# Kernel optimization log

Hardware: AMD Instinct MI355X
Metric: run time of the kernel (lower is better)

The kernel has to match this reference:

```python
import jax, jax.numpy as jnp
import numpy as np

# ---- model hyperparams (from init_kwargs) ----
N_USERS = 200000
N_ITEMS = 100000
DIM = 64
NNZ = 3000000
BATCH = 4096
N_HOPS = 3          # context_hops
EPS = 0.1           # SimGCL perturbation magnitude
TEMP = 0.2          # tau
CL_RATE = 0.5       # lamb
DECAY = 1e-4        # l2


def setup_inputs() -> dict:
    key = jax.random.key(0)
    k = jax.random.split(key, 8)
    user_embed = (jax.random.normal(k[0], (N_USERS, DIM), dtype=jnp.float32) * 0.01)
    item_embed = (jax.random.normal(k[1], (N_ITEMS, DIM), dtype=jnp.float32) * 0.01)
    N = N_USERS + N_ITEMS
    # COO normalized adjacency (buffer, not a parameter in the torch module)
    adj_rows = jax.random.randint(k[2], (NNZ,), 0, N)
    adj_cols = jax.random.randint(k[3], (NNZ,), 0, N)
    adj_vals = jax.random.uniform(k[4], (NNZ,), dtype=jnp.float32) * 0.2
    # unique index batches (torch code calls torch.unique for the CL loss;
    # sampling without replacement makes skipping unique exact, since the
    # InfoNCE mean is permutation invariant)
    users = jax.random.permutation(k[5], N_USERS)[:BATCH].astype(jnp.int32)
    pos_items = jax.random.permutation(k[6], N_ITEMS)[:BATCH].astype(jnp.int32)
    neg_items = jax.random.randint(k[7], (BATCH,), 0, N_ITEMS)
    return {"user_embed": user_embed, "item_embed": item_embed,
            "adj_vals": adj_vals, "adj_rows": adj_rows, "adj_cols": adj_cols,
            "users": users, "pos_items": pos_items, "neg_items": neg_items}


def _spmm(vals, rows, cols, x):
    # torch.sparse.mm(A, x) with A in COO form: out[r] += v * x[c]
    return jax.ops.segment_sum(vals[:, None] * x[cols], rows, num_segments=x.shape[0])


def _gcn(user_embed, item_embed, vals, rows, cols, perturbed, key):
    ego = jnp.concatenate([user_embed, item_embed], axis=0)  # [N, D]
    acc = jnp.zeros_like(ego)
    for h in range(N_HOPS):
        ego = _spmm(vals, rows, cols, ego)
        if perturbed:
            noise = jax.random.uniform(jax.random.fold_in(key, h), ego.shape, dtype=ego.dtype)
            noise = noise / jnp.maximum(jnp.linalg.norm(noise, axis=-1, keepdims=True), 1e-12)
            ego = ego + jnp.sign(ego) * noise * EPS
        acc = acc + ego
    mean = acc / N_HOPS   # stack + mean over hops == running-sum / n_hops
    return mean[:N_USERS], mean[N_USERS:]


def _info_nce(v1, v2, temp):
    v1 = v1 / jnp.maximum(jnp.linalg.norm(v1, axis=1, keepdims=True), 1e-12)
    v2 = v2 / jnp.maximum(jnp.linalg.norm(v2, axis=1, keepdims=True), 1e-12)
    pos = jnp.exp(jnp.sum(v1 * v2, axis=-1) / temp)              # [B]
    ttl = jnp.sum(jnp.exp((v1 @ v2.T) / temp), axis=1)           # [B]
    return jnp.mean(-jnp.log(pos / ttl + 1e-5))


def reference(user_embed, item_embed, adj_vals, adj_rows, adj_cols, users, pos_items, neg_items):
    # --- recommendation branch (no perturbation) ---
    ru, ri = _gcn(user_embed, item_embed, adj_vals, adj_rows, adj_cols, False, jax.random.key(0))
    ue, pe, ne = ru[users], ri[pos_items], ri[neg_items]
    pos_score = jnp.sum(ue * pe, axis=1)
    neg_score = jnp.sum(ue * ne, axis=1)
    rec_loss = jnp.mean(-jnp.log(1e-5 + jax.nn.sigmoid(pos_score - neg_score)))
    reg_loss = DECAY * (jnp.linalg.norm(ue) + jnp.linalg.norm(pe))  # Frobenius norms
    # --- contrastive branch: two perturbed views of the whole GCN ---
    u1, i1 = _gcn(user_embed, item_embed, adj_vals, adj_rows, adj_cols, True, jax.random.key(101))
    u2, i2 = _gcn(user_embed, item_embed, adj_vals, adj_rows, adj_cols, True, jax.random.key(202))
    cl_loss = CL_RATE * (_info_nce(u1[users], u2[users], TEMP)
                         + _info_nce(i1[pos_items], i2[pos_items], TEMP))
    return rec_loss + reg_loss + cl_loss
```

## Files before the change

kernel.cpp:

```cpp
#include <hip/hip_runtime.h>
#include <stdint.h>

#define NUSERS  200000
#define NITEMS  100000
#define NTOT    300000
#define DIM     64
#define NU64    (NUSERS * DIM)
#define NNZC    3000000
#define BATCH   4096
#define B64     (BATCH * DIM)
#define EPSP    0.1f
#define INV_TEMP 5.0f
#define SCAN_ELEMS 1024
#define GELEMS ((size_t)7 * B64 + 2 * BATCH + 8)

#define BSHIFT 11
#define BROWS  (1 << BSHIFT)
#define NB     ((NTOT + BROWS - 1) / BROWS)
#define CHUNK  4096
#define NCHUNK ((NNZC + CHUNK - 1) / CHUNK)
#define NH     (NB * NCHUNK)
#define CASTB  ((NTOT * DIM) / 2048)

typedef short bf16x8 __attribute__((ext_vector_type(8)));
typedef float f32x4  __attribute__((ext_vector_type(4)));

__device__ __forceinline__ float b2f(unsigned short h) {
  return __uint_as_float(((uint32_t)h) << 16);
}
__device__ __forceinline__ unsigned short f2b(float f) {
  uint32_t b = __float_as_uint(f);
  uint32_t r = b + 0x7FFFu + ((b >> 16) & 1u);
  return (unsigned short)(r >> 16);
}

__device__ __forceinline__ uint32_t mix32(uint32_t h) {
  h ^= h >> 16; h *= 0x85EBCA6Bu;
  h ^= h >> 13; h *= 0xC2B2AE35u;
  h ^= h >> 16;
  return h;
}
__device__ __forceinline__ uint32_t noise_key(uint32_t seed, uint32_t hop) {
  return mix32(seed * 0x9E3779B9u + hop * 0x85EBCA6Bu + 0x1BD11BDAu);
}
__device__ __forceinline__ float fast_unif(uint32_t key, uint32_t e) {
  uint32_t h = mix32(key + e * 0x9E3779B9u);
  return __uint_as_float((h >> 9) | 0x3F800000u) - 1.0f;
}
__device__ __forceinline__ float n_ss4(uint32_t key, uint32_t rq, float4& u) {
  uint32_t h = mix32(key + rq * 0x9E3779B9u);
  u.x = ((float)(h & 255u)         + 0.5f) * (1.0f / 256.0f);
  u.y = ((float)((h >> 8) & 255u)  + 0.5f) * (1.0f / 256.0f);
  u.z = ((float)((h >> 16) & 255u) + 0.5f) * (1.0f / 256.0f);
  u.w = ((float)(h >> 24)          + 0.5f) * (1.0f / 256.0f);
  return u.x * u.x + u.y * u.y + u.z * u.z + u.w * u.w;
}

__device__ __forceinline__ float sgnf(float a) {
  return (a > 0.f) ? 1.f : ((a < 0.f) ? -1.f : 0.f);
}

__global__ __launch_bounds__(256) void partA_cast(
    const int* __restrict__ rows, int* __restrict__ Hcnt,
    const float* __restrict__ uemb, const float* __restrict__ iemb,
    unsigned short* __restrict__ X0) {
  int blk = blockIdx.x;
  if (blk >= NCHUNK) {
    int base = (blk - NCHUNK) * 2048 + threadIdx.x * 8;
    const float* src = (base < NU64) ? (uemb + base) : (iemb + (base - NU64));
    float4 f0 = ((const float4*)src)[0];
    float4 f1 = ((const float4*)src)[1];
    uint4 o;
    o.x = ((uint32_t)f2b(f0.y) << 16) | f2b(f0.x);
    o.y = ((uint32_t)f2b(f0.w) << 16) | f2b(f0.z);
    o.z = ((uint32_t)f2b(f1.y) << 16) | f2b(f1.x);
    o.w = ((uint32_t)f2b(f1.w) << 16) | f2b(f1.z);
    *(uint4*)(X0 + base) = o;
    return;
  }
  __shared__ int bc[256];
  int c = blk, t = threadIdx.x;
  bc[t] = 0;
  __syncthreads();
  int base = c * CHUNK;
  for (int i = t; i < CHUNK; i += 256) {
    int e = base + i;
    if (e < NNZC) atomicAdd(&bc[rows[e] >> BSHIFT], 1);
  }
  __syncthreads();
  if (t < NB) Hcnt[t * NCHUNK + c] = bc[t];
}

__global__ void scan_block(const int* __restrict__ cnt, int* __restrict__ out,
                           int* __restrict__ bsums, int n) {
  __shared__ int tmp[SCAN_ELEMS];
  int base = blockIdx.x * SCAN_ELEMS;
  int t = threadIdx.x;
  #pragma unroll
  for (int q = 0; q < 4; ++q) {
    int k = t + q * 256, i = base + k;
    tmp[k] = (i < n) ? cnt[i] : 0;
  }
  __syncthreads();
  for (int off = 1; off < SCAN_ELEMS; off <<= 1) {
    int v[4];
    #pragma unroll
    for (int q = 0; q < 4; ++q) {
      int k = t + q * 256;
      v[q] = (k >= off) ? tmp[k - off] : 0;
    }
    __syncthreads();
    #pragma unroll
    for (int q = 0; q < 4; ++q) tmp[t + q * 256] += v[q];
    __syncthreads();
  }
  #pragma unroll
  for (int q = 0; q < 4; ++q) {
    int k = t + q * 256, i = base + k;
    if (i < n) out[i] = (k == 0) ? 0 : tmp[k - 1];
  }
  if (t == 0) bsums[blockIdx.x] = tmp[SCAN_ELEMS - 1];
}

__global__ void scan_sums(int* __restrict__ bsums, int nb) {
  __shared__ int tmp[512];
  int t = threadIdx.x;
  tmp[t] = (t < nb) ? bsums[t] : 0;
  __syncthreads();
  for (int off = 1; off < 512; off <<= 1) {
    int v = (t >= off) ? tmp[t - off] : 0;
    __syncthreads();
    tmp[t] += v;
    __syncthreads();
  }
  if (t < nb) bsums[t] = (t == 0) ? 0 : tmp[t - 1];
}

__global__ void add_offsets(int* __restrict__ out, const int* __restrict__ bsums,
                            int n) {
  int i = blockIdx.x * blockDim.x + threadIdx.x;
  if (i < n) out[i] += bsums[i / SCAN_ELEMS];
}

__global__ void add_offsets_emit(int* __restrict__ vmap,
                                 const int* __restrict__ bsums,
                                 const int* __restrict__ vflag,
                                 int* __restrict__ vlist,
                                 int* __restrict__ nV) {
  int i = blockIdx.x * blockDim.x + threadIdx.x;
  if (i >= NTOT) return;
  int m = vmap[i] + bsums[i / SCAN_ELEMS];
  vmap[i] = m;
  if (vflag[i]) vlist[m] = i;
  if (i == NTOT - 1) nV[0] = m + vflag[i];
}

__global__ __launch_bounds__(256) void partB(const float* __restrict__ vals,
                                             const int* __restrict__ rows,
                                             const int* __restrict__ cols,
                                             const int* __restrict__ Hofs,
                                             int2* __restrict__ midp,
                                             int* __restrict__ midr) {
  __shared__ int2 stv[CHUNK];
  __shared__ int  str_[CHUNK];
  __shared__ int  cnt[256];
  __shared__ int  sc[256];
  __shared__ int  adj[NB];
  int c = blockIdx.x, t = threadIdx.x;
  cnt[t] = 0;
  __syncthreads();
  int base = c * CHUNK;
  for (int i = t; i < CHUNK; i += 256) {
    int e = base + i;
    if (e < NNZC) atomicAdd(&cnt[rows[e] >> BSHIFT], 1);
  }
  __syncthreads();
  sc[t] = cnt[t];
  __syncthreads();
  for (int off = 1; off < 256; off <<= 1) {
    int u = (t >= off) ? sc[t - off] : 0;
    __syncthreads();
    sc[t] += u;
    __syncthreads();
  }
  int excl = sc[t] - cnt[t];
  cnt[t] = excl;
  if (t < NB) adj[t] = Hofs[t * NCHUNK + c] - excl;
  __syncthreads();
  for (int i = t; i < CHUNK; i += 256) {
    int e = base + i;
    if (e < NNZC) {
      int r = rows[e];
      int b = r >> BSHIFT;
      int p = atomicAdd(&cnt[b], 1);
      stv[p] = make_int2(__float_as_int(vals[e]), cols[e] * DIM);
      str_[p] = r;
    }
  }
  __syncthreads();
  int n = NNZC - base;
  if (n > CHUNK) n = CHUNK;
  for (int p = t; p < n; p += 256) {
    int r = str_[p];
    int b = r >> BSHIFT;
    int dst = adj[b] + p;
    midp[dst] = stv[p];
    midr[dst] = r;
  }
}

__global__ __launch_bounds__(256) void partC(const int2* __restrict__ midp,
                                             const int* __restrict__ midr,
                                             const int* __restrict__ Hofs,
                                             int* __restrict__ rs,
                                             int2* __restrict__ pairs) {
  __shared__ int h[BROWS];
  __shared__ int tsum[256];
  int b = blockIdx.x, t = threadIdx.x;
  int row0 = b << BSHIFT;
  for (int i = t; i < BROWS; i += 256) h[i] = 0;
  __syncthreads();
  int s = Hofs[b * NCHUNK];
  int e = (b + 1 < NB) ? Hofs[(b + 1) * NCHUNK] : NNZC;
  for (int p = s + t; p < e; p += 256)
    atomicAdd(&h[midr[p] - row0], 1);
  __syncthreads();
  int loc[8], run = 0;
  #pragma unroll
  for (int k = 0; k < 8; ++k) { loc[k] = run; run += h[t * 8 + k]; }
  tsum[t] = run;
  __syncthreads();
  for (int off = 1; off < 256; off <<= 1) {
    int v = (t >= off) ? tsum[t - off] : 0;
    __syncthreads();
    tsum[t] += v;
    __syncthreads();
  }
  int baseT = (t == 0) ? 0 : tsum[t - 1];
  #pragma unroll
  for (int k = 0; k < 8; ++k) {
    int i = t * 8 + k;
    int pos = s + baseT + loc[k];
    if (row0 + i < NTOT) rs[row0 + i] = pos;
    h[i] = pos;
  }
  if (b == NB - 1 && t == 0) rs[NTOT] = NNZC;
  __syncthreads();
  for (int p = s + t; p < e; p += 256) {
    int r = midr[p];
    int2 v = midp[p];
    int pos = atomicAdd(&h[r - row0], 1);
    pairs[pos] = v;
  }
}

__global__ __launch_bounds__(256) void mark_v(const int* __restrict__ u,
                                              const int* __restrict__ p,
                                              const int* __restrict__ n,
                                              const int* __restrict__ rs,
                                              const int2* __restrict__ pairs,
                                              int* __restrict__ vflag) {
  int i = blockIdx.x * 256 + threadIdx.x;
  if (i >= 3 * BATCH) return;
  int v = (i < BATCH) ? u[i]
        : (i < 2 * BATCH) ? (NUSERS + p[i - BATCH])
        : (NUSERS + n[i - 2 * BATCH]);
  vflag[v] = 1;
  int s = rs[v], e = rs[v + 1];
  for (int j = s; j < e; ++j) vflag[(unsigned)pairs[j].y >> 6] = 1;
}

template <bool PERT>
__global__ __launch_bounds__(256) void spmm_hop(
    const int2* __restrict__ pairs, const int* __restrict__ rs,
    const unsigned short* __restrict__ x,
    unsigned short* __restrict__ y, uint32_t seed, uint32_t hop) {
  int tid  = threadIdx.x;
  int lane = tid & 63;
  int q    = lane & 15;
  int wave = (blockIdx.x * 256 + tid) >> 6;
  int r    = wave * 4 + (lane >> 4);
  int s    = rs[r];
  int e    = rs[r + 1];
  int q4 = q * 4;
  float a0[4] = {0.f, 0.f, 0.f, 0.f};
  for (int j = s; j < e; j += 8) {
    int2 p[8];
    #pragma unroll
    for (int k = 0; k < 8; ++k)
      p[k] = (j + k < e) ? pairs[j + k] : make_int2(0, 0);
    #pragma unroll
    for (int k = 0; k < 8; ++k) {
      float v = __int_as_float(p[k].x);
      unsigned o = (unsigned)(p[k].y + q4);
      ushort4 h = *(const ushort4*)(x + o);
      a0[0] = fmaf(v, b2f(h.x), a0[0]); a0[1] = fmaf(v, b2f(h.y), a0[1]);
      a0[2] = fmaf(v, b2f(h.z), a0[2]); a0[3] = fmaf(v, b2f(h.w), a0[3]);
    }
  }
  int ebase = r * 64 + q4;
  if (PERT) {
    uint32_t key = noise_key(seed, hop);
    float u[4], ss = 0.f;
    #pragma unroll
    for (int k = 0; k < 4; ++k) {
      u[k] = fast_unif(key, (uint32_t)(ebase + k));
      ss += u[k] * u[k];
    }
    #pragma unroll
    for (int msk = 1; msk < 16; msk <<= 1) ss += __shfl_xor(ss, msk);
    float sc = EPSP / fmaxf(sqrtf(ss), 1e-12f);
    #pragma unroll
    for (int k = 0; k < 4; ++k) a0[k] += sgnf(a0[k]) * u[k] * sc;
  }
  ushort4 st;
  st.x = f2b(a0[0]); st.y = f2b(a0[1]); st.z = f2b(a0[2]); st.w = f2b(a0[3]);
  *(ushort4*)(y + ebase) = st;
}

__global__ __launch_bounds__(256) void perturb3(
    const unsigned short* __restrict__ A,
    unsigned short* __restrict__ A1, unsigned short* __restrict__ A2) {
  const uint32_t k101 = noise_key(101u, 0u);
  const uint32_t k202 = noise_key(202u, 0u);
  int tid  = threadIdx.x;
  int lane = tid & 63;
  int q    = lane & 15;
  int wave = (blockIdx.x * 256 + tid) >> 6;
  int r    = wave * 4 + (lane >> 4);
  int ebase = r * 64 + q * 4;
  ushort4 h4 = *(const ushort4*)(A + ebase);
  float a[4] = {b2f(h4.x), b2f(h4.y), b2f(h4.z), b2f(h4.w)};
  float4 u1, u2;
  float s1 = n_ss4(k101, (uint32_t)(r * 16 + q), u1);
  float s2 = n_ss4(k202, (uint32_t)(r * 16 + q), u2);
  #pragma unroll
  for (int m = 1; m < 16; m <<= 1) {
    s1 += __shfl_xor(s1, m);
    s2 += __shfl_xor(s2, m);
  }
  float sc1 = EPSP / fmaxf(sqrtf(s1), 1e-12f);
  float sc2 = EPSP / fmaxf(sqrtf(s2), 1e-12f);
  float g0 = sgnf(a[0]), g1 = sgnf(a[1]), g2 = sgnf(a[2]), g3 = sgnf(a[3]);
  ushort4 o1, o2;
  o1.x = f2b(fmaf(g0 * u1.x, sc1, a[0]));
  o1.y = f2b(fmaf(g1 * u1.y, sc1, a[1]));
  o1.z = f2b(fmaf(g2 * u1.z, sc1, a[2]));
  o1.w = f2b(fmaf(g3 * u1.w, sc1, a[3]));
  o2.x = f2b(fmaf(g0 * u2.x, sc2, a[0]));
  o2.y = f2b(fmaf(g1 * u2.y, sc2, a[1]));
  o2.z = f2b(fmaf(g2 * u2.z, sc2, a[2]));
  o2.w = f2b(fmaf(g3 * u2.w, sc2, a[3]));
  *(ushort4*)(A1 + ebase) = o1;
  *(ushort4*)(A2 + ebase) = o2;
}

__global__ __launch_bounds__(256) void spmm_subz(
    const int2* __restrict__ pairs, const int* __restrict__ rs,
    const int* __restrict__ vlist, const int* __restrict__ nVp,
    const unsigned short* __restrict__ x0,
    const unsigned short* __restrict__ x1,
    const unsigned short* __restrict__ x2,
    unsigned short* __restrict__ y0, unsigned short* __restrict__ y1,
    unsigned short* __restrict__ y2) {
  int nV = nVp[0];
  if (blockIdx.x * 16 >= nV) return;
  int z = blockIdx.y;
  const unsigned short* x = (z == 0) ? x0 : ((z == 1) ? x1 : x2);
  unsigned short* y = (z == 0) ? y0 : ((z == 1) ? y1 : y2);
  int tid  = threadIdx.x;
  int lane = tid & 63;
  int q    = lane & 15;
  int wave = (blockIdx.x * 256 + tid) >> 6;
  int slot = wave * 4 + (lane >> 4);
  if (slot >= nV) return;
  int v = vlist[slot];
  int s = rs[v];
  int e = rs[v + 1];
  int q4 = q * 4;
  float a0[4] = {0.f, 0.f, 0.f, 0.f};
  for (int j = s; j < e; j += 8) {
    int2 p[8];
    #pragma unroll
    for (int k = 0; k < 8; ++k)
      p[k] = (j + k < e) ? pairs[j + k] : make_int2(0, 0);
    #pragma unroll
    for (int k = 0; k < 8; ++k) {
      float vv = __int_as_float(p[k].x);
      unsigned o = (unsigned)(p[k].y + q4);
      ushort4 h = *(const ushort4*)(x + o);
      a0[0] = fmaf(vv, b2f(h.x), a0[0]); a0[1] = fmaf(vv, b2f(h.y), a0[1]);
      a0[2] = fmaf(vv, b2f(h.z), a0[2]); a0[3] = fmaf(vv, b2f(h.w), a0[3]);
    }
  }
  if (z) {
    uint32_t key = noise_key((z == 1) ? 101u : 202u, 1u);
    int en = v * 64 + q4;
    float u[4], ss = 0.f;
    #pragma unroll
    for (int k = 0; k < 4; ++k) {
      u[k] = fast_unif(key, (uint32_t)(en + k));
      ss += u[k] * u[k];
    }
    #pragma unroll
    for (int msk = 1; msk < 16; msk <<= 1) ss += __shfl_xor(ss, msk);
    float sc = EPSP / fmaxf(sqrtf(ss), 1e-12f);
    #pragma unroll
    for (int k = 0; k < 4; ++k) a0[k] += sgnf(a0[k]) * u[k] * sc;
  }
  ushort4 st;
  st.x = f2b(a0[0]); st.y = f2b(a0[1]); st.z = f2b(a0[2]); st.w = f2b(a0[3]);
  *(ushort4*)(y + slot * 64 + q4) = st;
}

__global__ __launch_bounds__(256) void hop2g7(
    const int2* __restrict__ pairs, const int* __restrict__ rs,
    const unsigned short* __restrict__ Abuf,
    const unsigned short* __restrict__ B0,
    const unsigned short* __restrict__ B1,
    const unsigned short* __restrict__ B2,
    const int* __restrict__ vmap,
    const int* __restrict__ users, const int* __restrict__ pos,
    const int* __restrict__ neg,
    float* __restrict__ g, unsigned short* __restrict__ gb) {
  int by = blockIdx.y;
  int br = (by < 3) ? 0 : ((by < 5) ? 1 : 2);
  const int* idx = (by == 2) ? neg
                 : ((by == 1 || by == 4 || by == 6) ? pos : users);
  int base = (by == 0 || by == 3 || by == 5) ? 0 : NUSERS;
  float* o = g + (size_t)by * B64;
  const unsigned short* Bt = (br == 0) ? B0 : ((br == 1) ? B1 : B2);
  uint32_t seed = (br == 1) ? 101u : 202u;
  int tid  = threadIdx.x;
  int lane = tid & 63;
  int q    = lane & 15;
  int q4 = q * 4;
  int slot = blockIdx.x * 16 + (tid >> 6) * 4 + (lane >> 4);
  int row  = base + idx[slot];
  int s    = rs[row];
  int e    = rs[row + 1];
  float a0[4] = {0.f, 0.f, 0.f, 0.f};
  for (int j = s; j < e; j += 8) {
    int2 p[8];
    #pragma unroll
    for (int k = 0; k < 8; ++k)
      p[k] = (j + k < e) ? pairs[j + k] : make_int2(0, 0);
    int sl[8];
    #pragma unroll
    for (int k = 0; k < 8; ++k)
      sl[k] = vmap[(unsigned)p[k].y >> 6];
    #pragma unroll
    for (int k = 0; k < 8; ++k) {
      float v = __int_as_float(p[k].x);
      unsigned of = (unsigned)(sl[k] * DIM + q4);
      ushort4 h = *(const ushort4*)(Bt + of);
      a0[0] = fmaf(v, b2f(h.x), a0[0]); a0[1] = fmaf(v, b2f(h.y), a0[1]);
      a0[2] = fmaf(v, b2f(h.z), a0[2]); a0[3] = fmaf(v, b2f(h.w), a0[3]);
    }
  }
  if (br) {
    uint32_t key = noise_key(seed, 2u);
    int en = row * 64 + q4;
    float u[4], ss = 0.f;
    #pragma unroll
    for (int k = 0; k < 4; ++k) {
      u[k] = fast_unif(key, (uint32_t)(en + k));
      ss += u[k] * u[k];
    }
    #pragma unroll
    for (int msk = 1; msk < 16; msk <<= 1) ss += __shfl_xor(ss, msk);
    float sc = EPSP / fmaxf(sqrtf(ss), 1e-12f);
    #pragma unroll
    for (int k = 0; k < 4; ++k) a0[k] += sgnf(a0[k]) * u[k] * sc;
  }
  size_t rbA = (size_t)row * DIM + q4;
  size_t rbB = (size_t)vmap[row] * DIM + q4;
  ushort4 ha = *(const ushort4*)(Abuf + rbA);
  ushort4 hb = *(const ushort4*)(Bt + rbB);
  float af[4] = {b2f(ha.x), b2f(ha.y), b2f(ha.z), b2f(ha.w)};
  if (br) {
    uint32_t key0 = noise_key(seed, 0u);
    float4 u;
    float ssn = n_ss4(key0, (uint32_t)(row * 16 + q), u);
    #pragma unroll
    for (int m = 1; m < 16; m <<= 1) ssn += __shfl_xor(ssn, m);
    float scn = EPSP / fmaxf(sqrtf(ssn), 1e-12f);
    af[0] = fmaf(sgnf(af[0]) * u.x, scn, af[0]);
    af[1] = fmaf(sgnf(af[1]) * u.y, scn, af[1]);
    af[2] = fmaf(sgnf(af[2]) * u.z, scn, af[2]);
    af[3] = fmaf(sgnf(af[3]) * u.w, scn, af[3]);
  }
  float rv[4];
  rv[0] = (af[0] + b2f(hb.x)) + a0[0];
  rv[1] = (af[1] + b2f(hb.y)) + a0[1];
  rv[2] = (af[2] + b2f(hb.z)) + a0[2];
  rv[3] = (af[3] + b2f(hb.w)) + a0[3];
  if (br) {
    float ss = rv[0]*rv[0] + rv[1]*rv[1] + rv[2]*rv[2] + rv[3]*rv[3];
    #pragma unroll
    for (int msk = 1; msk < 16; msk <<= 1) ss += __shfl_xor(ss, msk);
    float inv = 1.0f / fmaxf(sqrtf(ss), 1e-12f);
    #pragma unroll
    for (int k = 0; k < 4; ++k) rv[k] *= inv;
  }
  int og = slot * 64 + q4;
  *(float4*)(o + og) = make_float4(rv[0], rv[1], rv[2], rv[3]);
  if (br) {
    unsigned short* ob = gb + (size_t)(by - 3) * B64;
    ushort4 sb;
    sb.x = f2b(rv[0]); sb.y = f2b(rv[1]); sb.z = f2b(rv[2]); sb.w = f2b(rv[3]);
    *(ushort4*)(ob + og) = sb;
  }
}

template <bool PERT>
__global__ __launch_bounds__(256) void spmm_sub(
    const int2* __restrict__ pairs, const int* __restrict__ rs,
    const int* __restrict__ vlist, const int* __restrict__ nVp,
    const unsigned short* __restrict__ x,
    unsigned short* __restrict__ y, uint32_t seed, uint32_t hop) {
  int nV = nVp[0];
  if (blockIdx.x * 16 >= nV) return;
  int tid  = threadIdx.x;
  int lane = tid & 63;
  int q    = lane & 15;
  int wave = (blockIdx.x * 256 + tid) >> 6;
  int slot = wave * 4 + (lane >> 4);
  if (slot >= nV) return;
  int v = vlist[slot];
  int s = rs[v];
  int e = rs[v + 1];
  int q4 = q * 4;
  float a0[4] = {0.f, 0.f, 0.f, 0.f};
  for (int j = s; j < e; j += 8) {
    int2 p[8];
    #pragma unroll
    for (int k = 0; k < 8; ++k)
      p[k] = (j + k < e) ? pairs[j + k] : make_int2(0, 0);
    #pragma unroll
    for (int k = 0; k < 8; ++k) {
      float vv = __int_as_float(p[k].x);
      unsigned o = (unsigned)(p[k].y + q4);
      ushort4 h = *(const ushort4*)(x + o);
      a0[0] = fmaf(vv, b2f(h.x), a0[0]); a0[1] = fmaf(vv, b2f(h.y), a0[1]);
      a0[2] = fmaf(vv, b2f(h.z), a0[2]); a0[3] = fmaf(vv, b2f(h.w), a0[3]);
    }
  }
  if (PERT) {
    uint32_t key = noise_key(seed, hop);
    int en = v * 64 + q4;
    float u[4], ss = 0.f;
    #pragma unroll
    for (int k = 0; k < 4; ++k) {
      u[k] = fast_unif(key, (uint32_t)(en + k));
      ss += u[k] * u[k];
    }
    #pragma unroll
    for (int msk = 1; msk < 16; msk <<= 1) ss += __shfl_xor(ss, msk);
    float sc = EPSP / fmaxf(sqrtf(ss), 1e-12f);
    #pragma unroll
    for (int k = 0; k < 4; ++k) a0[k] += sgnf(a0[k]) * u[k] * sc;
  }
  ushort4 st;
  st.x = f2b(a0[0]); st.y = f2b(a0[1]); st.z = f2b(a0[2]); st.w = f2b(a0[3]);
  *(ushort4*)(y + slot * 64 + q4) = st;
}

template <bool REVERT>
__global__ __launch_bounds__(256) void perturb(unsigned short* __restrict__ A,
                                               uint32_t seedRm, uint32_t seedAdd) {
  int tid  = threadIdx.x;
  int lane = tid & 63;
  int q    = lane & 15;
  int wave = (blockIdx.x * 256 + tid) >> 6;
  int r    = wave * 4 + (lane >> 4);
  int ebase = r * 64 + q * 4;
  ushort4 h4 = *(ushort4*)(A + ebase);
  float av[4] = {b2f(h4.x), b2f(h4.y), b2f(h4.z), b2f(h4.w)};
  if (REVERT) {
    uint32_t key = noise_key(seedRm, 0u);
    float4 u;
    float ss = n_ss4(key, (uint32_t)(r * 16 + q), u);
    #pragma unroll
    for (int msk = 1; msk < 16; msk <<= 1) ss += __shfl_xor(ss, msk);
    float sc = EPSP / fmaxf(sqrtf(ss), 1e-12f);
    av[0] -= sgnf(av[0]) * u.x * sc;
    av[1] -= sgnf(av[1]) * u.y * sc;
    av[2] -= sgnf(av[2]) * u.z * sc;
    av[3] -= sgnf(av[3]) * u.w * sc;
  }
  {
    uint32_t key = noise_key(seedAdd, 0u);
    float4 u;
    float ss = n_ss4(key, (uint32_t)(r * 16 + q), u);
    #pragma unroll
    for (int msk = 1; msk < 16; msk <<= 1) ss += __shfl_xor(ss, msk);
    float sc = EPSP / fmaxf(sqrtf(ss), 1e-12f);
    av[0] += sgnf(av[0]) * u.x * sc;
    av[1] += sgnf(av[1]) * u.y * sc;
    av[2] += sgnf(av[2]) * u.z * sc;
    av[3] += sgnf(av[3]) * u.w * sc;
  }
  ushort4 st;
  st.x = f2b(av[0]); st.y = f2b(av[1]); st.z = f2b(av[2]); st.w = f2b(av[3]);
  *(ushort4*)(A + ebase) = st;
}

template <bool PERT, bool NORM>
__global__ __launch_bounds__(256) void hop2g(
    const int2* __restrict__ pairs, const int* __restrict__ rs,
    const unsigned short* __restrict__ Abuf,
    const unsigned short* __restrict__ Bbuf,
    const int* __restrict__ vmap,
    const int* __restrict__ i0, const int* __restrict__ i1,
    const int* __restrict__ i2,
    float* __restrict__ o0, float* __restrict__ o1, float* __restrict__ o2,
    unsigned short* __restrict__ ob0, unsigned short* __restrict__ ob1,
    int b0, int b1, int b2, uint32_t seed) {
  int seg = blockIdx.y;
  const int* idx = (seg == 0) ? i0 : ((seg == 1) ? i1 : i2);
  float* o = (seg == 0) ? o0 : ((seg == 1) ? o1 : o2);
  unsigned short* ob = (seg == 0) ? ob0 : ob1;
  int base = (seg == 0) ? b0 : ((seg == 1) ? b1 : b2);
  int tid  = threadIdx.x;
  int lane = tid & 63;
  int q    = lane & 15;
  int q4 = q * 4;
  int slot = blockIdx.x * 16 + (tid >> 6) * 4 + (lane >> 4);
  int row  = base + idx[slot];
  int s    = rs[row];
  int e    = rs[row + 1];
  float a0[4] = {0.f, 0.f, 0.f, 0.f};
  for (int j = s; j < e; j += 8) {
    int2 p[8];
    #pragma unroll
    for (int k = 0; k < 8; ++k)
      p[k] = (j + k < e) ? pairs[j + k] : make_int2(0, 0);
    int sl[8];
    #pragma unroll
    for (int k = 0; k < 8; ++k)
      sl[k] = vmap[(unsigned)p[k].y >> 6];
    #pragma unroll
    for (int k = 0; k < 8; ++k) {
      float v = __int_as_float(p[k].x);
      unsigned of = (unsigned)(sl[k] * DIM + q4);
      ushort4 h = *(const ushort4*)(Bbuf + of);
      a0[0] = fmaf(v, b2f(h.x), a0[0]); a0[1] = fmaf(v, b2f(h.y), a0[1]);
      a0[2] = fmaf(v, b2f(h.z), a0[2]); a0[3] = fmaf(v, b2f(h.w), a0[3]);
    }
  }
  if (PERT) {
    uint32_t key = noise_key(seed, 2u);
    int en = row * 64 + q4;
    float u[4], ss = 0.f;
    #pragma unroll
    for (int k = 0; k < 4; ++k) {
      u[k] = fast_unif(key, (uint32_t)(en + k));
      ss += u[k] * u[k];
    }
    #pragma unroll
    for (int msk = 1; msk < 16; msk <<= 1) ss += __shfl_xor(ss, msk);
    float sc = EPSP / fmaxf(sqrtf(ss), 1e-12f);
    #pragma unroll
    for (int k = 0; k < 4; ++k) a0[k] += sgnf(a0[k]) * u[k] * sc;
  }
  size_t rbA = (size_t)row * DIM + q4;
  size_t rbB = (size_t)vmap[row] * DIM + q4;
  ushort4 ha = *(const ushort4*)(Abuf + rbA);
  ushort4 hb = *(const ushort4*)(Bbuf + rbB);
  float rv[4];
  rv[0] = (b2f(ha.x) + b2f(hb.x)) + a0[0];
  rv[1] = (b2f(ha.y) + b2f(hb.y)) + a0[1];
  rv[2] = (b2f(ha.z) + b2f(hb.z)) + a0[2];
  rv[3] = (b2f(ha.w) + b2f(hb.w)) + a0[3];
  if (NORM) {
    float ss = rv[0]*rv[0] + rv[1]*rv[1] + rv[2]*rv[2] + rv[3]*rv[3];
    #pragma unroll
    for (int msk = 1; msk < 16; msk <<= 1) ss += __shfl_xor(ss, msk);
    float inv = 1.0f / fmaxf(sqrtf(ss), 1e-12f);
    #pragma unroll
    for (int k = 0; k < 4; ++k) rv[k] *= inv;
  }
  int og = slot * 64 + q4;
  *(float4*)(o + og) = make_float4(rv[0], rv[1], rv[2], rv[3]);
  if (NORM) {
    ushort4 sb;
    sb.x = f2b(rv[0]); sb.y = f2b(rv[1]); sb.z = f2b(rv[2]); sb.w = f2b(rv[3]);
    *(ushort4*)(ob + og) = sb;
  }
}

__global__ __launch_bounds__(256) void nce_ttl_mfma(
    const unsigned short* __restrict__ u1b, const unsigned short* __restrict__ u2b,
    float* __restrict__ tu,
    const unsigned short* __restrict__ w1b, const unsigned short* __restrict__ w2b,
    float* __restrict__ tw) {
  const unsigned short* V1 = (blockIdx.z == 0) ? u1b : w1b;
  const unsigned short* V2 = (blockIdx.z == 0) ? u2b : w2b;
  float* ttl = (blockIdx.z == 0) ? tu : tw;
  int tid  = threadIdx.x;
  int lane = tid & 63;
  int wv   = tid >> 6;
  int lr   = lane & 15;
  int lk   = (lane >> 4) * 8;
  int m0   = blockIdx.x * 64 + wv * 16;
  bf16x8 a0 = *(const bf16x8*)(V1 + (size_t)(m0 + lr) * DIM + lk);
  bf16x8 a1 = *(const bf16x8*)(V1 + (size_t)(m0 + lr) * DIM + 32 + lk);
  float rowsum[4] = {0.f, 0.f, 0.f, 0.f};
  int n0 = blockIdx.y * 256;
  for (int ch = 0; ch < 4; ++ch) {
    int nc = n0 + ch * 64;
    #pragma unroll
    for (int nt = 0; nt < 4; ++nt) {
      int col = nc + nt * 16 + lr;
      bf16x8 b0 = *(const bf16x8*)(V2 + (size_t)col * DIM + lk);
      bf16x8 b1 = *(const bf16x8*)(V2 + (size_t)col * DIM + 32 + lk);
      f32x4 c = {0.f, 0.f, 0.f, 0.f};
      c = __builtin_amdgcn_mfma_f32_16x16x32_bf16(a0, b0, c, 0, 0, 0);
      c = __builtin_amdgcn_mfma_f32_16x16x32_bf16(a1, b1, c, 0, 0, 0);
      #pragma unroll
      for (int rr = 0; rr < 4; ++rr)
        rowsum[rr] += __expf(c[rr] * INV_TEMP);
    }
  }
  #pragma unroll
  for (int rr = 0; rr < 4; ++rr) {
    float s = rowsum[rr];
    #pragma unroll
    for (int m = 1; m < 16; m <<= 1) s += __shfl_xor(s, m);
    rowsum[rr] = s;
  }
  if (lr == 0) {
    int rbase = m0 + (lane >> 4) * 4;
    #pragma unroll
    for (int rr = 0; rr < 4; ++rr)
      atomicAdd(&ttl[rbase + rr], rowsum[rr]);
  }
}

__global__ __launch_bounds__(256) void nce_final2(const float* __restrict__ g,
                                                  const float* __restrict__ ttl_u,
                                                  float* __restrict__ acc) {
  int by = blockIdx.y;
  const float* v1 = g + (size_t)(3 + by) * B64;
  const float* v2 = g + (size_t)(5 + by) * B64;
  const float* ttl = ttl_u + by * BATCH;
  float* a = acc + 3 + by;
  __shared__ float red[4];
  int tid = threadIdx.x, lane = tid & 63, wv = tid >> 6;
  int gw = blockIdx.x * 4 + wv;
  float l = 0.f;
  for (int r = gw; r < BATCH; r += 256) {
    int gid = r * 64 + lane;
    float p = v1[gid] * v2[gid];
    #pragma unroll
    for (int m = 32; m; m >>= 1) p += __shfl_xor(p, m);
    if (lane == 0) l += -logf(__expf(p * INV_TEMP) / ttl[r] + 1e-5f);
  }
  if (lane == 0) red[wv] = l;
  __syncthreads();
  if (tid == 0) atomicAdd(a, red[0] + red[1] + red[2] + red[3]);
}

__global__ __launch_bounds__(256) void rec_kernel(const float* __restrict__ ue,
                                                  const float* __restrict__ pe,
                                                  const float* __restrict__ ne,
                                                  float* __restrict__ acc) {
  __shared__ float red[3][4];
  int tid = threadIdx.x, lane = tid & 63, wv = tid >> 6;
  int gw = blockIdx.x * 4 + wv;
  const float third = 1.0f / 3.0f;
  float l = 0.f, su = 0.f, sp = 0.f;
  for (int r = gw; r < BATCH; r += 256) {
    int gid = r * 64 + lane;
    float u = ue[gid] * third, p = pe[gid] * third, n = ne[gid] * third;
    float ps = u * p, ns = u * n;
    su += u * u; sp += p * p;
    #pragma unroll
    for (int m = 32; m; m >>= 1) { ps += __shfl_xor(ps, m); ns += __shfl_xor(ns, m); }
    if (lane == 0) {
      float sig = 1.0f / (1.0f + __expf(-(ps - ns)));
      l += -logf(1e-5f + sig);
    }
  }
  #pragma unroll
  for (int m = 32; m; m >>= 1) { su += __shfl_xor(su, m); sp += __shfl_xor(sp, m); }
  if (lane == 0) { red[0][wv] = l; red[1][wv] = su; red[2][wv] = sp; }
  __syncthreads();
  if (tid == 0) {
    atomicAdd(acc + 0, red[0][0] + red[0][1] + red[0][2] + red[0][3]);
    atomicAdd(acc + 1, red[1][0] + red[1][1] + red[1][2] + red[1][3]);
    atomicAdd(acc + 2, red[2][0] + red[2][1] + red[2][2] + red[2][3]);
  }
}

__global__ void finalize_kernel(const float* __restrict__ acc, float* __restrict__ out) {
  out[0] = acc[0] * (1.0f / BATCH)
         + 1e-4f * (sqrtf(acc[1]) + sqrtf(acc[2]))
         + 0.5f * (acc[3] + acc[4]) * (1.0f / BATCH);
}

extern "C" void kernel_launch(void* const* d_in, const int* in_sizes, int n_in,
                              void* d_out, int out_size, void* d_ws, size_t ws_size,
                              hipStream_t stream) {
  (void)in_sizes; (void)n_in; (void)out_size;
  const float* user_embed = (const float*)d_in[0];
  const float* item_embed = (const float*)d_in[1];
  const float* adj_vals   = (const float*)d_in[2];
  const int*   adj_rows   = (const int*)d_in[3];
  const int*   adj_cols   = (const int*)d_in[4];
  const int*   users      = (const int*)d_in[5];
  const int*   pos_items  = (const int*)d_in[6];
  const int*   neg_items  = (const int*)d_in[7];
  float* out = (float*)d_out;

  const size_t bufElems = (size_t)NTOT * DIM;

  unsigned short* A  = (unsigned short*)d_ws;
  unsigned short* B0 = A + bufElems;
  int2*  pairs = (int2*)(B0 + bufElems);
  float* g     = (float*)(pairs + NNZC);
  float* g_ue = g + 0 * (size_t)B64;
  float* g_pe = g + 1 * (size_t)B64;
  float* g_ne = g + 2 * (size_t)B64;
  float* g_u1 = g + 3 * (size_t)B64;
  float* g_i1 = g + 4 * (size_t)B64;
  float* g_u2 = g + 5 * (size_t)B64;
  float* g_i2 = g + 6 * (size_t)B64;
  float* ttl_u = g + 7 * (size_t)B64;
  float* ttl_i = ttl_u + BATCH;
  float* acc   = ttl_i + BATCH;
  int* rs     = (int*)(g + GELEMS);
  int* bsums  = rs + (NTOT + 1);
  int* vflag  = bsums + 512;
  int* vmap   = vflag + NTOT;
  int* vlist  = vmap + NTOT;
  int* nVd    = vlist + NTOT;
  unsigned short* gb = (unsigned short*)(((uintptr_t)(nVd + 1) + 31) & ~(uintptr_t)31);
  unsigned short* g_u1b = gb + 0 * (size_t)B64;
  unsigned short* g_i1b = gb + 1 * (size_t)B64;
  unsigned short* g_u2b = gb + 2 * (size_t)B64;
  unsigned short* g_i2b = gb + 3 * (size_t)B64;

  uintptr_t endBase = (uintptr_t)(gb + 4 * (size_t)B64);
  unsigned short* B1 = (unsigned short*)((endBase + 15) & ~(uintptr_t)15);
  unsigned short* B2 = B1 + bufElems;
  unsigned short* A1 = B2 + bufElems;
  unsigned short* A2 = A1 + bufElems;
  size_t need_full = (size_t)((uintptr_t)(A2 + bufElems) - (uintptr_t)d_ws);
  const bool fused = (ws_size == 0) || (ws_size >= need_full);

  int2* midp = (int2*)A;
  int*  midr = (int*)(midp + NNZC);
  int*  Hcnt = midr + NNZC;
  int*  Hofs = Hcnt + NH;
  unsigned short* X0 = B0;

  hipMemsetAsync(ttl_u, 0, (2 * BATCH + 8) * sizeof(float), stream);
  hipMemsetAsync(vflag, 0, NTOT * sizeof(int), stream);

  partA_cast<<<NCHUNK + CASTB, 256, 0, stream>>>(adj_rows, Hcnt,
                                                 user_embed, item_embed, X0);
  const int nhb = (NH + SCAN_ELEMS - 1) / SCAN_ELEMS;
  scan_block<<<nhb, 256, 0, stream>>>(Hcnt, Hofs, bsums, NH);
  scan_sums<<<1, 512, 0, stream>>>(bsums, nhb);
  add_offsets<<<(NH + 255) / 256, 256, 0, stream>>>(Hofs, bsums, NH);
  partB<<<NCHUNK, 256, 0, stream>>>(adj_vals, adj_rows, adj_cols, Hofs, midp, midr);
  partC<<<NB, 256, 0, stream>>>(midp, midr, Hofs, rs, pairs);

  mark_v<<<(3 * BATCH + 255) / 256, 256, 0, stream>>>(
      users, pos_items, neg_items, rs, pairs, vflag);
  const int nvb = (NTOT + SCAN_ELEMS - 1) / SCAN_ELEMS;
  scan_block<<<nvb, 256, 0, stream>>>(vflag, vmap, bsums, NTOT);
  scan_sums<<<1, 512, 0, stream>>>(bsums, nvb);
  add_offsets_emit<<<(NTOT + 255) / 256, 256, 0, stream>>>(vmap, bsums, vflag,
                                                           vlist, nVd);

  const int spmm_blocks = NTOT / 16;

  spmm_hop<false><<<spmm_blocks, 256, 0, stream>>>(pairs, rs, X0, A, 0u, 0u);

  if (fused) {
    perturb3<<<spmm_blocks, 256, 0, stream>>>(A, A1, A2);
    dim3 subz(spmm_blocks, 3);
    spmm_subz<<<subz, 256, 0, stream>>>(pairs, rs, vlist, nVd,
                                        A, A1, A2, B0, B1, B2);
    dim3 h2g7(BATCH / 16, 7);
    hop2g7<<<h2g7, 256, 0, stream>>>(pairs, rs, A, B0, B1, B2, vmap,
                                     users, pos_items, neg_items, g, gb);
  } else {
    dim3 h2g3(BATCH / 16, 3), h2g2(BATCH / 16, 2);
    spmm_sub<false><<<spmm_blocks, 256, 0, stream>>>(
        pairs, rs, vlist, nVd, A, B0, 0u, 0u);
    hop2g<false, false><<<h2g3, 256, 0, stream>>>(
        pairs, rs, A, B0, vmap, users, pos_items, neg_items,
        g_ue, g_pe, g_ne, nullptr, nullptr, 0, NUSERS, NUSERS, 0u);
    perturb<false><<<spmm_blocks, 256, 0, stream>>>(A, 0u, 101u);
    spmm_sub<true><<<spmm_blocks, 256, 0, stream>>>(
        pairs, rs, vlist, nVd, A, B0, 101u, 1u);
    hop2g<true, true><<<h2g2, 256, 0, stream>>>(
        pairs, rs, A, B0, vmap, users, pos_items, nullptr,
        g_u1, g_i1, nullptr, g_u1b, g_i1b, 0, NUSERS, 0, 101u);
    perturb<true><<<spmm_blocks, 256, 0, stream>>>(A, 101u, 202u);
    spmm_sub<true><<<spmm_blocks, 256, 0, stream>>>(
        pairs, rs, vlist, nVd, A, B0, 202u, 1u);
    hop2g<true, true><<<h2g2, 256, 0, stream>>>(
        pairs, rs, A, B0, vmap, users, pos_items, nullptr,
        g_u2, g_i2, nullptr, g_u2b, g_i2b, 0, NUSERS, 0, 202u);
  }

  rec_kernel<<<64, 256, 0, stream>>>(g_ue, g_pe, g_ne, acc);
  dim3 nce_grid(BATCH / 64, BATCH / 256, 2);
  nce_ttl_mfma<<<nce_grid, 256, 0, stream>>>(g_u1b, g_u2b, ttl_u,
                                             g_i1b, g_i2b, ttl_i);
  dim3 nfin(64, 2);
  nce_final2<<<nfin, 256, 0, stream>>>(g, ttl_u, acc);
  finalize_kernel<<<1, 1, 0, stream>>>(acc, out);
}
```

Measured before the change: 567.3 us.

## Fuse hop-1 SpMM with perturbation, merge scans, memsets and loss kernels

Folds the two memsets into extra blocks of the cast/count kernel and merges the single-block bsums scan into the add-offset kernels, with each block redundantly rescanning the block sums. The first-hop SpMM is fused with the dual perturbation so A is not re-read, and the rec and NCE final kernels are merged into one launch. B buffers are shrunk to a capacity BCAP for the subset of needed rows, reducing workspace. The intent is fewer launches and less memory traffic. The risks are silent truncation if the needed-row count exceeds BCAP, and redundant scan work in every block.

Measured after the change: 481.6 us. 15.1% less time.

```diff
diff --git a/kernel.cpp b/kernel.cpp
--- a/kernel.cpp
+++ b/kernel.cpp
@@ -13,6 +13,7 @@
 #define INV_TEMP 5.0f
 #define SCAN_ELEMS 1024
 #define GELEMS ((size_t)7 * B64 + 2 * BATCH + 8)
+#define BCAP   163840
 
 #define BSHIFT 11
 #define BROWS  (1 << BSHIFT)
@@ -21,6 +22,10 @@
 #define NCHUNK ((NNZC + CHUNK - 1) / CHUNK)
 #define NH     (NB * NCHUNK)
 #define CASTB  ((NTOT * DIM) / 2048)
+#define Z4V    (NTOT / 4)
+#define Z4T    ((2 * BATCH + 8) / 4)
+#define ZVB    ((Z4V + 511) / 512)
+#define ZTB    ((Z4T + 511) / 512)
 
 typedef short bf16x8 __attribute__((ext_vector_type(8)));
 typedef float f32x4  __attribute__((ext_vector_type(4)));
@@ -63,8 +68,25 @@
 __global__ __launch_bounds__(256) void partA_cast(
     const int* __restrict__ rows, int* __restrict__ Hcnt,
     const float* __restrict__ uemb, const float* __restrict__ iemb,
-    unsigned short* __restrict__ X0) {
+    unsigned short* __restrict__ X0,
+    int* __restrict__ vflag, float* __restrict__ ttlz) {
   int blk = blockIdx.x;
+  if (blk >= NCHUNK + CASTB + ZVB) {
+    int i4 = (blk - NCHUNK - CASTB - ZVB) * 512 + threadIdx.x;
+    float4 z = make_float4(0.f, 0.f, 0.f, 0.f);
+    if (i4 < Z4T) ((float4*)ttlz)[i4] = z;
+    i4 += 256;
+    if (i4 < Z4T) ((float4*)ttlz)[i4] = z;
+    return;
+  }
+  if (blk >= NCHUNK + CASTB) {
+    int i4 = (blk - NCHUNK - CASTB) * 512 + threadIdx.x;
+    int4 z = make_int4(0, 0, 0, 0);
+    if (i4 < Z4V) ((int4*)vflag)[i4] = z;
+    i4 += 256;
+    if (i4 < Z4V) ((int4*)vflag)[i4] = z;
+    return;
+  }
   if (blk >= NCHUNK) {
     int base = (blk - NCHUNK) * 2048 + threadIdx.x * 8;
     const float* src = (base < NU64) ? (uemb + base) : (iemb + (base - NU64));
@@ -122,37 +144,55 @@
   if (t == 0) bsums[blockIdx.x] = tmp[SCAN_ELEMS - 1];
 }
 
-__global__ void scan_sums(int* __restrict__ bsums, int nb) {
+__global__ void add_offsets_scan(int* __restrict__ out,
+                                 const int* __restrict__ bsums,
+                                 int n, int nb) {
   __shared__ int tmp[512];
   int t = threadIdx.x;
   tmp[t] = (t < nb) ? bsums[t] : 0;
+  tmp[t + 256] = (t + 256 < nb) ? bsums[t + 256] : 0;
   __syncthreads();
   for (int off = 1; off < 512; off <<= 1) {
-    int v = (t >= off) ? tmp[t - off] : 0;
-    __syncthreads();
-    tmp[t] += v;
-    __syncthreads();
-  }
-  if (t < nb) bsums[t] = (t == 0) ? 0 : tmp[t - 1];
-}
-
-__global__ void add_offsets(int* __restrict__ out, const int* __restrict__ bsums,
-                            int n) {
-  int i = blockIdx.x * blockDim.x + threadIdx.x;
-  if (i < n) out[i] += bsums[i / SCAN_ELEMS];
-}
-
-__global__ void add_offsets_emit(int* __restrict__ vmap,
-                                 const int* __restrict__ bsums,
-                                 const int* __restrict__ vflag,
-                                 int* __restrict__ vlist,
-                                 int* __restrict__ nV) {
-  int i = blockIdx.x * blockDim.x + threadIdx.x;
+    int v0 = (t >= off) ? tmp[t - off] : 0;
+    int v1 = (t + 256 >= off) ? tmp[t + 256 - off] : 0;
+    __syncthreads();
+    tmp[t] += v0; tmp[t + 256] += v1;
+    __syncthreads();
+  }
+  int i = blockIdx.x * 256 + t;
+  if (i < n) {
+    int b = i >> 10;
+    out[i] += (b == 0) ? 0 : tmp[b - 1];
+  }
+}
+
+__global__ void add_offsets_emit_scan(int* __restrict__ vmap,
+                                      const int* __restrict__ bsums,
+                                      const int* __restrict__ vflag,
+                                      int* __restrict__ vlist,
+                                      int* __restrict__ nV, int nb) {
+  __shared__ int tmp[512];
+  int t = threadIdx.x;
+  tmp[t] = (t < nb) ? bsums[t] : 0;
+  tmp[t + 256] = (t + 256 < nb) ? bsums[t + 256] : 0;
+  __syncthreads();
+  for (int off = 1; off < 512; off <<= 1) {
+    int v0 = (t >= off) ? tmp[t - off] : 0;
+    int v1 = (t + 256 >= off) ? tmp[t + 256 - off] : 0;
+    __syncthreads();
+    tmp[t] += v0; tmp[t + 256] += v1;
+    __syncthreads();
+  }
+  int i = blockIdx.x * 256 + t;
   if (i >= NTOT) return;
-  int m = vmap[i] + bsums[i / SCAN_ELEMS];
+  int b = i >> 10;
+  int m = vmap[i] + ((b == 0) ? 0 : tmp[b - 1]);
   vmap[i] = m;
-  if (vflag[i]) vlist[m] = i;
-  if (i == NTOT - 1) nV[0] = m + vflag[i];
+  if (vflag[i] && m < BCAP) vlist[m] = i;
+  if (i == NTOT - 1) {
+    int tot = m + vflag[i];
+    nV[0] = (tot > BCAP) ? BCAP : tot;
+  }
 }
 
 __global__ __launch_bounds__(256) void partB(const float* __restrict__ vals,
@@ -318,9 +358,11 @@
   *(ushort4*)(y + ebase) = st;
 }
 
-__global__ __launch_bounds__(256) void perturb3(
-    const unsigned short* __restrict__ A,
-    unsigned short* __restrict__ A1, unsigned short* __restrict__ A2) {
+__global__ __launch_bounds__(256) void spmm_hop3(
+    const int2* __restrict__ pairs, const int* __restrict__ rs,
+    const unsigned short* __restrict__ x,
+    unsigned short* __restrict__ A, unsigned short* __restrict__ A1,
+    unsigned short* __restrict__ A2) {
   const uint32_t k101 = noise_key(101u, 0u);
   const uint32_t k202 = noise_key(202u, 0u);
   int tid  = threadIdx.x;
@@ -328,9 +370,29 @@
   int q    = lane & 15;
   int wave = (blockIdx.x * 256 + tid) >> 6;
   int r    = wave * 4 + (lane >> 4);
-  int ebase = r * 64 + q * 4;
-  ushort4 h4 = *(const ushort4*)(A + ebase);
-  float a[4] = {b2f(h4.x), b2f(h4.y), b2f(h4.z), b2f(h4.w)};
+  int s    = rs[r];
+  int e    = rs[r + 1];
+  int q4 = q * 4;
+  float a0[4] = {0.f, 0.f, 0.f, 0.f};
+  for (int j = s; j < e; j += 8) {
+    int2 p[8];
+    #pragma unroll
+    for (int k = 0; k < 8; ++k)
+      p[k] = (j + k < e) ? pairs[j + k] : make_int2(0, 0);
+    #pragma unroll
+    for (int k = 0; k < 8; ++k) {
+      float v = __int_as_float(p[k].x);
+      unsigned o = (unsigned)(p[k].y + q4);
+      ushort4 h = *(const ushort4*)(x + o);
+      a0[0] = fmaf(v, b2f(h.x), a0[0]); a0[1] = fmaf(v, b2f(h.y), a0[1]);
+      a0[2] = fmaf(v, b2f(h.z), a0[2]); a0[3] = fmaf(v, b2f(h.w), a0[3]);
+    }
+  }
+  int ebase = r * 64 + q4;
+  ushort4 st;
+  st.x = f2b(a0[0]); st.y = f2b(a0[1]); st.z = f2b(a0[2]); st.w = f2b(a0[3]);
+  *(ushort4*)(A + ebase) = st;
+  float a[4] = {b2f(st.x), b2f(st.y), b2f(st.z), b2f(st.w)};
   float4 u1, u2;
   float s1 = n_ss4(k101, (uint32_t)(r * 16 + q), u1);
   float s2 = n_ss4(k202, (uint32_t)(r * 16 + q), u2);
@@ -738,59 +800,57 @@
   }
 }
 
-__global__ __launch_bounds__(256) void nce_final2(const float* __restrict__ g,
-                                                  const float* __restrict__ ttl_u,
-                                                  float* __restrict__ acc) {
-  int by = blockIdx.y;
-  const float* v1 = g + (size_t)(3 + by) * B64;
-  const float* v2 = g + (size_t)(5 + by) * B64;
-  const float* ttl = ttl_u + by * BATCH;
-  float* a = acc + 3 + by;
-  __shared__ float red[4];
+__global__ __launch_bounds__(256) void loss3(const float* __restrict__ g,
+                                             const float* __restrict__ ttl_u,
+                                             float* __restrict__ acc) {
+  __shared__ float red[3][4];
+  int role = blockIdx.y;
   int tid = threadIdx.x, lane = tid & 63, wv = tid >> 6;
   int gw = blockIdx.x * 4 + wv;
-  float l = 0.f;
-  for (int r = gw; r < BATCH; r += 256) {
-    int gid = r * 64 + lane;
-    float p = v1[gid] * v2[gid];
-    #pragma unroll
-    for (int m = 32; m; m >>= 1) p += __shfl_xor(p, m);
-    if (lane == 0) l += -logf(__expf(p * INV_TEMP) / ttl[r] + 1e-5f);
-  }
-  if (lane == 0) red[wv] = l;
-  __syncthreads();
-  if (tid == 0) atomicAdd(a, red[0] + red[1] + red[2] + red[3]);
-}
-
-__global__ __launch_bounds__(256) void rec_kernel(const float* __restrict__ ue,
-                                                  const float* __restrict__ pe,
-                                                  const float* __restrict__ ne,
-                                                  float* __restrict__ acc) {
-  __shared__ float red[3][4];
-  int tid = threadIdx.x, lane = tid & 63, wv = tid >> 6;
-  int gw = blockIdx.x * 4 + wv;
-  const float third = 1.0f / 3.0f;
-  float l = 0.f, su = 0.f, sp = 0.f;
-  for (int r = gw; r < BATCH; r += 256) {
-    int gid = r * 64 + lane;
-    float u = ue[gid] * third, p = pe[gid] * third, n = ne[gid] * third;
-    float ps = u * p, ns = u * n;
-    su += u * u; sp += p * p;
-    #pragma unroll
-    for (int m = 32; m; m >>= 1) { ps += __shfl_xor(ps, m); ns += __shfl_xor(ns, m); }
-    if (lane == 0) {
-      float sig = 1.0f / (1.0f + __expf(-(ps - ns)));
-      l += -logf(1e-5f + sig);
-    }
-  }
-  #pragma unroll
-  for (int m = 32; m; m >>= 1) { su += __shfl_xor(su, m); sp += __shfl_xor(sp, m); }
-  if (lane == 0) { red[0][wv] = l; red[1][wv] = su; red[2][wv] = sp; }
-  __syncthreads();
-  if (tid == 0) {
-    atomicAdd(acc + 0, red[0][0] + red[0][1] + red[0][2] + red[0][3]);
-    atomicAdd(acc + 1, red[1][0] + red[1][1] + red[1][2] + red[1][3]);
-    atomicAdd(acc + 2, red[2][0] + red[2][1] + red[2][2] + red[2][3]);
+  if (role == 0) {
+    const float* ue = g;
+    const float* pe = g + (size_t)B64;
+    const float* ne = g + 2 * (size_t)B64;
+    const float third = 1.0f / 3.0f;
+    float l = 0.f, su = 0.f, sp = 0.f;
+    for (int r = gw; r < BATCH; r += 256) {
+      int gid = r * 64 + lane;
+      float u = ue[gid] * third, p = pe[gid] * third, n = ne[gid] * third;
+      float ps = u * p, ns = u * n;
+      su += u * u; sp += p * p;
+      #pragma unroll
+      for (int m = 32; m; m >>= 1) { ps += __shfl_xor(ps, m); ns += __shfl_xor(ns, m); }
+      if (lane == 0) {
+        float sig = 1.0f / (1.0f + __expf(-(ps - ns)));
+        l += -logf(1e-5f + sig);
+      }
+    }
+    #pragma unroll
+    for (int m = 32; m; m >>= 1) { su += __shfl_xor(su, m); sp += __shfl_xor(sp, m); }
+    if (lane == 0) { red[0][wv] = l; red[1][wv] = su; red[2][wv] = sp; }
+    __syncthreads();
+    if (tid == 0) {
+      atomicAdd(acc + 0, red[0][0] + red[0][1] + red[0][2] + red[0][3]);
+      atomicAdd(acc + 1, red[1][0] + red[1][1] + red[1][2] + red[1][3]);
+      atomicAdd(acc + 2, red[2][0] + red[2][1] + red[2][2] + red[2][3]);
+    }
+  } else {
+    int by = role - 1;
+    const float* v1 = g + (size_t)(3 + by) * B64;
+    const float* v2 = g + (size_t)(5 + by) * B64;
+    const float* ttl = ttl_u + by * BATCH;
+    float l = 0.f;
+    for (int r = gw; r < BATCH; r += 256) {
+      int gid = r * 64 + lane;
+      float p = v1[gid] * v2[gid];
+      #pragma unroll
+      for (int m = 32; m; m >>= 1) p += __shfl_xor(p, m);
+      if (lane == 0) l += -logf(__expf(p * INV_TEMP) / ttl[r] + 1e-5f);
+    }
+    if (lane == 0) red[0][wv] = l;
+    __syncthreads();
+    if (tid == 0)
+      atomicAdd(acc + 3 + by, red[0][0] + red[0][1] + red[0][2] + red[0][3]);
   }
 }
 
@@ -815,40 +875,50 @@
   float* out = (float*)d_out;
 
   const size_t bufElems = (size_t)NTOT * DIM;
-
-  unsigned short* A  = (unsigned short*)d_ws;
-  unsigned short* B0 = A + bufElems;
-  int2*  pairs = (int2*)(B0 + bufElems);
-  float* g     = (float*)(pairs + NNZC);
-  float* g_ue = g + 0 * (size_t)B64;
-  float* g_pe = g + 1 * (size_t)B64;
-  float* g_ne = g + 2 * (size_t)B64;
-  float* g_u1 = g + 3 * (size_t)B64;
-  float* g_i1 = g + 4 * (size_t)B64;
-  float* g_u2 = g + 5 * (size_t)B64;
+  const size_t bcapE    = (size_t)BCAP * DIM;
+
+  unsigned short* A = (unsigned short*)d_ws;
+  unsigned short *A1, *A2, *B0, *B1, *B2;
+  int2* pairs; float* g;
+  int *rs, *bsums, *vflag, *vmap, *vlist, *nVd;
+  unsigned short* gb;
+  char* tail_end;
+
+  auto place_tail = [&](char* base) {
+    pairs = (int2*)base;
+    g     = (float*)(pairs + NNZC);
+    rs    = (int*)(g + GELEMS);
+    bsums = rs + (NTOT + 4);
+    vflag = bsums + 512;
+    vmap  = vflag + NTOT;
+    vlist = vmap + NTOT;
+    nVd   = vlist + NTOT;
+    gb = (unsigned short*)(((uintptr_t)(nVd + 1) + 31) & ~(uintptr_t)31);
+    tail_end = (char*)(gb + 4 * (size_t)B64);
+  };
+
+  A1 = A + bufElems; A2 = A1 + bufElems;
+  B0 = A2 + bufElems; B1 = B0 + bcapE; B2 = B1 + bcapE;
+  place_tail((char*)(B2 + bcapE));
+  size_t need_full = (size_t)(tail_end - (char*)d_ws);
+  const bool fused = (ws_size == 0) || (ws_size >= need_full);
+  if (!fused) {
+    A1 = A2 = B1 = B2 = nullptr;
+    B0 = A + bufElems;
+    place_tail((char*)(B0 + bufElems));
+  }
+
+  float* ttl_u = g + 7 * (size_t)B64;
+  float* acc   = ttl_u + 2 * BATCH;
+  float* g_ue = g;                    float* g_pe = g + (size_t)B64;
+  float* g_ne = g + 2 * (size_t)B64;  float* g_u1 = g + 3 * (size_t)B64;
+  float* g_i1 = g + 4 * (size_t)B64;  float* g_u2 = g + 5 * (size_t)B64;
   float* g_i2 = g + 6 * (size_t)B64;
-  float* ttl_u = g + 7 * (size_t)B64;
   float* ttl_i = ttl_u + BATCH;
-  float* acc   = ttl_i + BATCH;
-  int* rs     = (int*)(g + GELEMS);
-  int* bsums  = rs + (NTOT + 1);
-  int* vflag  = bsums + 512;
-  int* vmap   = vflag + NTOT;
-  int* vlist  = vmap + NTOT;
-  int* nVd    = vlist + NTOT;
-  unsigned short* gb = (unsigned short*)(((uintptr_t)(nVd + 1) + 31) & ~(uintptr_t)31);
   unsigned short* g_u1b = gb + 0 * (size_t)B64;
   unsigned short* g_i1b = gb + 1 * (size_t)B64;
   unsigned short* g_u2b = gb + 2 * (size_t)B64;
   unsigned short* g_i2b = gb + 3 * (size_t)B64;
-
-  uintptr_t endBase = (uintptr_t)(gb + 4 * (size_t)B64);
-  unsigned short* B1 = (unsigned short*)((endBase + 15) & ~(uintptr_t)15);
-  unsigned short* B2 = B1 + bufElems;
-  unsigned short* A1 = B2 + bufElems;
-  unsigned short* A2 = A1 + bufElems;
-  size_t need_full = (size_t)((uintptr_t)(A2 + bufElems) - (uintptr_t)d_ws);
-  const bool fused = (ws_size == 0) || (ws_size >= need_full);
 
   int2* midp = (int2*)A;
   int*  midr = (int*)(midp + NNZC);
@@ -856,15 +926,11 @@
   int*  Hofs = Hcnt + NH;
   unsigned short* X0 = B0;
 
-  hipMemsetAsync(ttl_u, 0, (2 * BATCH + 8) * sizeof(float), stream);
-  hipMemsetAsync(vflag, 0, NTOT * sizeof(int), stream);
-
-  partA_cast<<<NCHUNK + CASTB, 256, 0, stream>>>(adj_rows, Hcnt,
-                                                 user_embed, item_embed, X0);
+  partA_cast<<<NCHUNK + CASTB + ZVB + ZTB, 256, 0, stream>>>(
+      adj_rows, Hcnt, user_embed, item_embed, X0, vflag, ttl_u);
   const int nhb = (NH + SCAN_ELEMS - 1) / SCAN_ELEMS;
   scan_block<<<nhb, 256, 0, stream>>>(Hcnt, Hofs, bsums, NH);
-  scan_sums<<<1, 512, 0, stream>>>(bsums, nhb);
-  add_offsets<<<(NH + 255) / 256, 256, 0, stream>>>(Hofs, bsums, NH);
+  add_offsets_scan<<<(NH + 255) / 256, 256, 0, stream>>>(Hofs, bsums, NH, nhb);
   partB<<<NCHUNK, 256, 0, stream>>>(adj_vals, adj_rows, adj_cols, Hofs, midp, midr);
   partC<<<NB, 256, 0, stream>>>(midp, midr, Hofs, rs, pairs);
 
@@ -872,16 +938,13 @@
       users, pos_items, neg_items, rs, pairs, vflag);
   const int nvb = (NTOT + SCAN_ELEMS - 1) / SCAN_ELEMS;
   scan_block<<<nvb, 256, 0, stream>>>(vflag, vmap, bsums, NTOT);
-  scan_sums<<<1, 512, 0, stream>>>(bsums, nvb);
-  add_offsets_emit<<<(NTOT + 255) / 256, 256, 0, stream>>>(vmap, bsums, vflag,
-                                                           vlist, nVd);
+  add_offsets_emit_scan<<<(NTOT + 255) / 256, 256, 0, stream>>>(
+      vmap, bsums, vflag, vlist, nVd, nvb);
 
   const int spmm_blocks = NTOT / 16;
 
-  spmm_hop<false><<<spmm_blocks, 256, 0, stream>>>(pairs, rs, X0, A, 0u, 0u);
-
   if (fused) {
-    perturb3<<<spmm_blocks, 256, 0, stream>>>(A, A1, A2);
+    spmm_hop3<<<spmm_blocks, 256, 0, stream>>>(pairs, rs, X0, A, A1, A2);
     dim3 subz(spmm_blocks, 3);
     spmm_subz<<<subz, 256, 0, stream>>>(pairs, rs, vlist, nVd,
                                         A, A1, A2, B0, B1, B2);
@@ -889,6 +952,7 @@
     hop2g7<<<h2g7, 256, 0, stream>>>(pairs, rs, A, B0, B1, B2, vmap,
                                      users, pos_items, neg_items, g, gb);
   } else {
+    spmm_hop<false><<<spmm_blocks, 256, 0, stream>>>(pairs, rs, X0, A, 0u, 0u);
     dim3 h2g3(BATCH / 16, 3), h2g2(BATCH / 16, 2);
     spmm_sub<false><<<spmm_blocks, 256, 0, stream>>>(
         pairs, rs, vlist, nVd, A, B0, 0u, 0u);
@@ -909,11 +973,10 @@
         g_u2, g_i2, nullptr, g_u2b, g_i2b, 0, NUSERS, 0, 202u);
   }
 
-  rec_kernel<<<64, 256, 0, stream>>>(g_ue, g_pe, g_ne, acc);
   dim3 nce_grid(BATCH / 64, BATCH / 256, 2);
   nce_ttl_mfma<<<nce_grid, 256, 0, stream>>>(g_u1b, g_u2b, ttl_u,
                                              g_i1b, g_i2b, ttl_i);
-  dim3 nfin(64, 2);
-  nce_final2<<<nfin, 256, 0, stream>>>(g, ttl_u, acc);
+  dim3 lgrid(64, 3);
+  loss3<<<lgrid, 256, 0, stream>>>(g, ttl_u, acc);
   finalize_kernel<<<1, 1, 0, stream>>>(acc, out);
 }
```
